# Optimization experiments

Hardware: AMD Instinct MI355X
Metric: run time of the kernel (lower is better)

Reference implementation:

```python
import jax, jax.numpy as jnp
import numpy as np

DIM = 512
N_HEADS = 8
HEAD_DIM = DIM // N_HEADS
TAU = 0.5
LN_EPS = 1e-5
B, L = 16, 8192


def setup_inputs() -> dict:
    key = jax.random.key(0)
    ks = jax.random.split(key, 12)
    s = 1.0 / np.sqrt(DIM)
    return {
        "Q": jax.random.normal(ks[0], (B, DIM), jnp.float32),
        "K": jax.random.normal(ks[1], (B, L, DIM), jnp.float32),
        "V": jax.random.normal(ks[2], (B, L, DIM), jnp.float32),
        "Wq": jax.random.normal(ks[3], (DIM, DIM), jnp.float32) * s,
        "bq": jnp.zeros((DIM,), jnp.float32),
        "Wk": jax.random.normal(ks[4], (DIM, DIM), jnp.float32) * s,
        "bk": jnp.zeros((DIM,), jnp.float32),
        "Wv": jax.random.normal(ks[5], (DIM, DIM), jnp.float32) * s,
        "bv": jnp.zeros((DIM,), jnp.float32),
        "Wo": jax.random.normal(ks[6], (DIM, DIM), jnp.float32) * s,
        "bo": jnp.zeros((DIM,), jnp.float32),
        "gamma": jnp.ones((DIM,), jnp.float32),
        "beta": jnp.zeros((DIM,), jnp.float32),
    }


def _layer_norm(x, gamma, beta):
    mu = jnp.mean(x, axis=-1, keepdims=True)
    var = jnp.var(x, axis=-1, keepdims=True)
    return (x - mu) * jax.lax.rsqrt(var + LN_EPS) * gamma + beta


def reference(Q, K, V, Wq, bq, Wk, bk, Wv, bv, Wo, bo, gamma, beta):
    Bsz = Q.shape[0]
    # projections
    q = (Q @ Wq + bq).reshape(Bsz, N_HEADS, HEAD_DIM)            # b h d
    k = (K @ Wk + bk).reshape(Bsz, -1, N_HEADS, HEAD_DIM)        # b l h d
    v = (V @ Wv + bv).reshape(Bsz, -1, N_HEADS, HEAD_DIM)        # b l h d
    # scaled dot-product score: single query per head
    scores = jnp.einsum("bhd,blhd->bhl", q, k) / np.sqrt(HEAD_DIM)
    # 'exp' simplex projection = temperature softmax
    weights = jax.nn.softmax(scores / TAU, axis=-1)              # b h l
    ctx = jnp.einsum("bhl,blhd->bhd", weights, v).reshape(Bsz, DIM)
    out = ctx @ Wo + bo                                          # n_heads != 1
    out = _layer_norm(out, gamma, beta)
    return out + Q
```

## Files before the change

kernel.cpp:

```cpp
#include <hip/hip_runtime.h>
#include <math.h>

#define DIM 512
#define NH 8
#define HD 64
#define LSEQ 8192
#define BSZ 16


__global__ __launch_bounds__(256) void k_qproj(const float* __restrict__ Q,
        const float* __restrict__ Wq, const float* __restrict__ bq,
        float* __restrict__ q) {
    int b = blockIdx.x >> 1;
    int j = ((blockIdx.x & 1) << 8) + threadIdx.x;
    __shared__ float qs[DIM];
    qs[threadIdx.x]       = Q[b * DIM + threadIdx.x];
    qs[threadIdx.x + 256] = Q[b * DIM + threadIdx.x + 256];
    __syncthreads();
    float acc = bq[j];
    #pragma unroll 8
    for (int i = 0; i < DIM; ++i) acc = fmaf(qs[i], Wq[i * DIM + j], acc);
    q[b * DIM + j] = acc;
}

__global__ __launch_bounds__(256) void k_tproj(const float* __restrict__ q,
        const float* __restrict__ Wk, float* __restrict__ t) {
    int b = blockIdx.x >> 4;
    int o = ((blockIdx.x & 15) << 8) + threadIdx.x;
    int h = o >> 9, i = o & 511;
    __shared__ float qs[DIM];
    qs[threadIdx.x]       = q[b * DIM + threadIdx.x];
    qs[threadIdx.x + 256] = q[b * DIM + threadIdx.x + 256];
    __syncthreads();
    const float* wk = Wk + (size_t)i * DIM + h * HD;
    const float* qh = qs + h * HD;
    float a = 0.f;
    #pragma unroll
    for (int j = 0; j < HD; ++j) a = fmaf(wk[j], qh[j], a);
    t[(b * NH + h) * DIM + i] = 0.25f * a;
}

__global__ __launch_bounds__(256) void k_scores(const float* __restrict__ Kin,
        const float* __restrict__ t, float* __restrict__ sc) {
    int b  = blockIdx.x >> 8;
    int l0 = (blockIdx.x & 255) << 5;
    int lane = threadIdx.x & 63;
    int wave = threadIdx.x >> 6;
    float4 ta[NH], tb[NH];
    #pragma unroll
    for (int h = 0; h < NH; ++h) {
        const float* tp = t + (b * NH + h) * DIM + lane * 8;
        ta[h] = *(const float4*)tp;
        tb[h] = *(const float4*)(tp + 4);
    }
    int lbase = l0 + wave * 8;
    float keep = 0.f;
    #pragma unroll
    for (int i = 0; i < 8; ++i) {
        const float* kp = Kin + ((size_t)(b * LSEQ + lbase + i)) * DIM + lane * 8;
        float4 ka = *(const float4*)kp;
        float4 kb = *(const float4*)(kp + 4);
        float s[NH];
        #pragma unroll
        for (int h = 0; h < NH; ++h) {
            float p = ka.x * ta[h].x + ka.y * ta[h].y + ka.z * ta[h].z + ka.w * ta[h].w
                    + kb.x * tb[h].x + kb.y * tb[h].y + kb.z * tb[h].z + kb.w * tb[h].w;
            p += __shfl_xor(p, 1);
            p += __shfl_xor(p, 2);
            p += __shfl_xor(p, 4);
            p += __shfl_xor(p, 8);
            p += __shfl_xor(p, 16);
            p += __shfl_xor(p, 32);
            s[h] = p;
        }
        int hh = lane >> 3;
        float sel = s[0];
        sel = (hh == 1) ? s[1] : sel;
        sel = (hh == 2) ? s[2] : sel;
        sel = (hh == 3) ? s[3] : sel;
        sel = (hh == 4) ? s[4] : sel;
        sel = (hh == 5) ? s[5] : sel;
        sel = (hh == 6) ? s[6] : sel;
        sel = (hh == 7) ? s[7] : sel;
        if ((lane & 7) == i) keep = sel;
    }
    int h = lane >> 3, i = lane & 7;
    sc[(size_t)(b * NH + h) * LSEQ + lbase + i] = keep;
}

__global__ __launch_bounds__(256) void k_softmax(float* __restrict__ sc) {
    float* base = sc + (size_t)blockIdx.x * LSEQ;
    int tid = threadIdx.x;
    int lane = tid & 63, wave = tid >> 6;
    float4 v[8];
    float m = -1e30f;
    #pragma unroll
    for (int k = 0; k < 8; ++k) {
        v[k] = *(const float4*)(base + tid * 4 + k * 1024);
        m = fmaxf(m, fmaxf(fmaxf(v[k].x, v[k].y), fmaxf(v[k].z, v[k].w)));
    }
    #pragma unroll
    for (int d = 1; d < 64; d <<= 1) m = fmaxf(m, __shfl_xor(m, d));
    __shared__ float sm[4], ss[4];
    if (lane == 0) sm[wave] = m;
    __syncthreads();
    m = fmaxf(fmaxf(sm[0], sm[1]), fmaxf(sm[2], sm[3]));
    float sum = 0.f;
    #pragma unroll
    for (int k = 0; k < 8; ++k) {
        v[k].x = __expf(v[k].x - m);
        v[k].y = __expf(v[k].y - m);
        v[k].z = __expf(v[k].z - m);
        v[k].w = __expf(v[k].w - m);
        sum += v[k].x + v[k].y + v[k].z + v[k].w;
    }
    #pragma unroll
    for (int d = 1; d < 64; d <<= 1) sum += __shfl_xor(sum, d);
    if (lane == 0) ss[wave] = sum;
    __syncthreads();
    sum = ss[0] + ss[1] + ss[2] + ss[3];
    float inv = 1.f / sum;
    #pragma unroll
    for (int k = 0; k < 8; ++k) {
        v[k].x *= inv; v[k].y *= inv; v[k].z *= inv; v[k].w *= inv;
        *(float4*)(base + tid * 4 + k * 1024) = v[k];
    }
}

__global__ __launch_bounds__(256) void k_vpass(const float* __restrict__ Vin,
        const float* __restrict__ sc, float* __restrict__ part) {
    int b = blockIdx.x >> 5;
    int chunk = blockIdx.x & 31;
    int l0 = chunk << 8;
    int tid = threadIdx.x;
    __shared__ float smem[4096];
    #pragma unroll
    for (int idx = tid; idx < 2048; idx += 256) {
        int h = idx >> 8, j = idx & 255;
        smem[j * 8 + h] = sc[(size_t)(b * NH + h) * LSEQ + l0 + j];
    }
    __syncthreads();
    int r = tid >> 7;
    int col = (tid & 127) << 2;
    float4 a0 = {0,0,0,0}, a1 = {0,0,0,0}, a2 = {0,0,0,0}, a3 = {0,0,0,0};
    float4 a4 = {0,0,0,0}, a5 = {0,0,0,0}, a6 = {0,0,0,0}, a7 = {0,0,0,0};
    #pragma unroll 4
    for (int j = r; j < 256; j += 2) {
        const float* vp = Vin + ((size_t)(b * LSEQ + l0 + j)) * DIM + col;
        float4 vv = *(const float4*)vp;
        float4 wa = *(const float4*)&smem[j * 8];
        float4 wb = *(const float4*)&smem[j * 8 + 4];
        a0.x = fmaf(wa.x, vv.x, a0.x); a0.y = fmaf(wa.x, vv.y, a0.y);
        a0.z = fmaf(wa.x, vv.z, a0.z); a0.w = fmaf(wa.x, vv.w, a0.w);
        a1.x = fmaf(wa.y, vv.x, a1.x); a1.y = fmaf(wa.y, vv.y, a1.y);
        a1.z = fmaf(wa.y, vv.z, a1.z); a1.w = fmaf(wa.y, vv.w, a1.w);
        a2.x = fmaf(wa.z, vv.x, a2.x); a2.y = fmaf(wa.z, vv.y, a2.y);
        a2.z = fmaf(wa.z, vv.z, a2.z); a2.w = fmaf(wa.z, vv.w, a2.w);
        a3.x = fmaf(wa.w, vv.x, a3.x); a3.y = fmaf(wa.w, vv.y, a3.y);
        a3.z = fmaf(wa.w, vv.z, a3.z); a3.w = fmaf(wa.w, vv.w, a3.w);
        a4.x = fmaf(wb.x, vv.x, a4.x); a4.y = fmaf(wb.x, vv.y, a4.y);
        a4.z = fmaf(wb.x, vv.z, a4.z); a4.w = fmaf(wb.x, vv.w, a4.w);
        a5.x = fmaf(wb.y, vv.x, a5.x); a5.y = fmaf(wb.y, vv.y, a5.y);
        a5.z = fmaf(wb.y, vv.z, a5.z); a5.w = fmaf(wb.y, vv.w, a5.w);
        a6.x = fmaf(wb.z, vv.x, a6.x); a6.y = fmaf(wb.z, vv.y, a6.y);
        a6.z = fmaf(wb.z, vv.z, a6.z); a6.w = fmaf(wb.z, vv.w, a6.w);
        a7.x = fmaf(wb.w, vv.x, a7.x); a7.y = fmaf(wb.w, vv.y, a7.y);
        a7.z = fmaf(wb.w, vv.z, a7.z); a7.w = fmaf(wb.w, vv.w, a7.w);
    }
    __syncthreads();
    if (r == 1) {
        *(float4*)&smem[0 * DIM + col] = a0; *(float4*)&smem[1 * DIM + col] = a1;
        *(float4*)&smem[2 * DIM + col] = a2; *(float4*)&smem[3 * DIM + col] = a3;
        *(float4*)&smem[4 * DIM + col] = a4; *(float4*)&smem[5 * DIM + col] = a5;
        *(float4*)&smem[6 * DIM + col] = a6; *(float4*)&smem[7 * DIM + col] = a7;
    }
    __syncthreads();
    if (r == 0) {
        float* pout = part + (size_t)(b * 32 + chunk) * 4096;
        float4 o;
        #define EMIT(H, A) \
            o = *(const float4*)&smem[H * DIM + col]; \
            o.x += A.x; o.y += A.y; o.z += A.z; o.w += A.w; \
            *(float4*)&pout[H * DIM + col] = o;
        EMIT(0, a0) EMIT(1, a1) EMIT(2, a2) EMIT(3, a3)
        EMIT(4, a4) EMIT(5, a5) EMIT(6, a6) EMIT(7, a7)
        #undef EMIT
    }
}

__global__ __launch_bounds__(256) void k_ureduce(const float* __restrict__ part,
        float* __restrict__ u) {
    int o = blockIdx.x * 256 + threadIdx.x;
    int b = o >> 12, rr = o & 4095;
    float s = 0.f;
    #pragma unroll 8
    for (int c = 0; c < 32; ++c) s += part[(size_t)(b * 32 + c) * 4096 + rr];
    u[o] = s;
}

__global__ __launch_bounds__(256) void k_ctx(const float* __restrict__ u,
        const float* __restrict__ Wv, const float* __restrict__ bv,
        float* __restrict__ ctx) {
    int b = blockIdx.x >> 1;
    int j = ((blockIdx.x & 1) << 8) + threadIdx.x;
    __shared__ float us[4096];
    for (int idx = threadIdx.x; idx < 4096; idx += 256) us[idx] = u[b * 4096 + idx];
    __syncthreads();
    int h = j >> 6;
    const float* uh = us + h * DIM;
    float a = bv[j];
    #pragma unroll 8
    for (int i = 0; i < DIM; ++i) a = fmaf(uh[i], Wv[(size_t)i * DIM + j], a);
    ctx[b * DIM + j] = a;
}

__global__ __launch_bounds__(256) void k_out(const float* __restrict__ ctx,
        const float* __restrict__ Wo, const float* __restrict__ bo,
        const float* __restrict__ gamma, const float* __restrict__ beta,
        const float* __restrict__ Qin, float* __restrict__ out) {
    int b = blockIdx.x;
    int tid = threadIdx.x;
    __shared__ float cs[DIM];
    cs[tid]       = ctx[b * DIM + tid];
    cs[tid + 256] = ctx[b * DIM + tid + 256];
    __syncthreads();
    float o0 = bo[tid], o1 = bo[tid + 256];
    #pragma unroll 8
    for (int m = 0; m < DIM; ++m) {
        float c = cs[m];
        o0 = fmaf(c, Wo[m * DIM + tid], o0);
        o1 = fmaf(c, Wo[m * DIM + tid + 256], o1);
    }
    float s = o0 + o1, sq = o0 * o0 + o1 * o1;
    #pragma unroll
    for (int d = 1; d < 64; d <<= 1) { s += __shfl_xor(s, d); sq += __shfl_xor(sq, d); }
    __shared__ float rs[4], rq[4];
    int lane = tid & 63, wave = tid >> 6;
    if (lane == 0) { rs[wave] = s; rq[wave] = sq; }
    __syncthreads();
    s  = rs[0] + rs[1] + rs[2] + rs[3];
    sq = rq[0] + rq[1] + rq[2] + rq[3];
    float mu = s * (1.f / DIM);
    float var = sq * (1.f / DIM) - mu * mu;
    float rstd = rsqrtf(var + 1e-5f);
    int j0 = tid, j1 = tid + 256;
    out[b * DIM + j0] = (o0 - mu) * rstd * gamma[j0] + beta[j0] + Qin[b * DIM + j0];
    out[b * DIM + j1] = (o1 - mu) * rstd * gamma[j1] + beta[j1] + Qin[b * DIM + j1];
}

extern "C" void kernel_launch(void* const* d_in, const int* in_sizes, int n_in,
                              void* d_out, int out_size, void* d_ws, size_t ws_size,
                              hipStream_t stream) {
    const float* Q     = (const float*)d_in[0];
    const float* K     = (const float*)d_in[1];
    const float* V     = (const float*)d_in[2];
    const float* Wq    = (const float*)d_in[3];
    const float* bq    = (const float*)d_in[4];
    const float* Wk    = (const float*)d_in[5];
    const float* Wv    = (const float*)d_in[7];
    const float* bv    = (const float*)d_in[8];
    const float* Wo    = (const float*)d_in[9];
    const float* bo    = (const float*)d_in[10];
    const float* gamma = (const float*)d_in[11];
    const float* beta  = (const float*)d_in[12];
    float* ws   = (float*)d_ws;
    float* q    = ws;
    float* t    = ws + 8192;
    float* sc   = ws + 73728;
    float* part = ws + 1122304;
    float* u    = ws + 3219456;
    float* ctx  = ws + 3284992;
    float* out  = (float*)d_out;

    k_qproj  <<<32,   256, 0, stream>>>(Q, Wq, bq, q);
    k_tproj  <<<256,  256, 0, stream>>>(q, Wk, t);
    k_scores <<<4096, 256, 0, stream>>>(K, t, sc);
    k_softmax<<<128,  256, 0, stream>>>(sc);
    k_vpass  <<<512,  256, 0, stream>>>(V, sc, part);
    k_ureduce<<<256,  256, 0, stream>>>(part, u);
    k_ctx    <<<32,   256, 0, stream>>>(u, Wv, bv, ctx);
    k_out    <<<16,   256, 0, stream>>>(ctx, Wo, bo, gamma, beta, Q, out);
}
```

Baseline: 643.4 us.

## Fuse scores, softmax and V pass into one flash-style attention kernel

Merges score computation, softmax and the weighted V sum into a single kernel per 128-row chunk. Each chunk keeps its local max and sum, and a later kernel rescales and combines the chunks. This removes the score round-trip to global memory and several launches. The Q and T projections are fused per (batch, head), and the output projection is split over K-slices with a separate LayerNorm kernel to expose more parallelism. Risks include fewer blocks in the attention kernel and the extra partial storage and merge cost.

```diff
diff --git a/kernel.cpp b/kernel.cpp
--- a/kernel.cpp
+++ b/kernel.cpp
@@ -6,150 +6,136 @@
 #define HD 64
 #define LSEQ 8192
 #define BSZ 16
-
-
-__global__ __launch_bounds__(256) void k_qproj(const float* __restrict__ Q,
+#define CHUNK 128
+#define NCH 64
+#define PSTRIDE 4112
+
+
+__global__ __launch_bounds__(256) void k_qt(const float* __restrict__ Q,
         const float* __restrict__ Wq, const float* __restrict__ bq,
-        float* __restrict__ q) {
-    int b = blockIdx.x >> 1;
-    int j = ((blockIdx.x & 1) << 8) + threadIdx.x;
-    __shared__ float qs[DIM];
-    qs[threadIdx.x]       = Q[b * DIM + threadIdx.x];
-    qs[threadIdx.x + 256] = Q[b * DIM + threadIdx.x + 256];
-    __syncthreads();
-    float acc = bq[j];
-    #pragma unroll 8
-    for (int i = 0; i < DIM; ++i) acc = fmaf(qs[i], Wq[i * DIM + j], acc);
-    q[b * DIM + j] = acc;
-}
-
-__global__ __launch_bounds__(256) void k_tproj(const float* __restrict__ q,
-        const float* __restrict__ Wk, float* __restrict__ t) {
-    int b = blockIdx.x >> 4;
-    int o = ((blockIdx.x & 15) << 8) + threadIdx.x;
-    int h = o >> 9, i = o & 511;
-    __shared__ float qs[DIM];
-    qs[threadIdx.x]       = q[b * DIM + threadIdx.x];
-    qs[threadIdx.x + 256] = q[b * DIM + threadIdx.x + 256];
-    __syncthreads();
-    const float* wk = Wk + (size_t)i * DIM + h * HD;
-    const float* qh = qs + h * HD;
-    float a = 0.f;
+        const float* __restrict__ Wk, float* __restrict__ t_g) {
+    int b = blockIdx.x >> 3, h = blockIdx.x & 7;
+    int tid = threadIdx.x;
+    __shared__ __align__(16) float qs[DIM];
+    __shared__ __align__(16) float partial[256];
+    __shared__ __align__(16) float qh[HD];
+    qs[tid]       = Q[b * DIM + tid];
+    qs[tid + 256] = Q[b * DIM + tid + 256];
+    __syncthreads();
+    int jj = tid & 63, ks = tid >> 6;
+    {
+        float a = 0.f;
+        const float* wp = Wq + (size_t)(ks * 128) * DIM + h * HD + jj;
+        const float* qp = qs + ks * 128;
+        #pragma unroll 8
+        for (int i = 0; i < 128; ++i) a = fmaf(qp[i], wp[(size_t)i * DIM], a);
+        partial[tid] = a;
+    }
+    __syncthreads();
+    if (tid < 64)
+        qh[tid] = partial[tid] + partial[tid + 64] + partial[tid + 128] +
+                  partial[tid + 192] + bq[h * HD + tid];
+    __syncthreads();
     #pragma unroll
-    for (int j = 0; j < HD; ++j) a = fmaf(wk[j], qh[j], a);
-    t[(b * NH + h) * DIM + i] = 0.25f * a;
-}
-
-__global__ __launch_bounds__(256) void k_scores(const float* __restrict__ Kin,
-        const float* __restrict__ t, float* __restrict__ sc) {
-    int b  = blockIdx.x >> 8;
-    int l0 = (blockIdx.x & 255) << 5;
-    int lane = threadIdx.x & 63;
-    int wave = threadIdx.x >> 6;
-    float4 ta[NH], tb[NH];
+    for (int rep = 0; rep < 2; ++rep) {
+        int i = tid + rep * 256;
+        const float4* wk = (const float4*)(Wk + (size_t)i * DIM + h * HD);
+        float a = 0.f;
+        #pragma unroll
+        for (int v = 0; v < 16; ++v) {
+            float4 w4 = wk[v];
+            a = fmaf(w4.x, qh[v * 4 + 0], a);
+            a = fmaf(w4.y, qh[v * 4 + 1], a);
+            a = fmaf(w4.z, qh[v * 4 + 2], a);
+            a = fmaf(w4.w, qh[v * 4 + 3], a);
+        }
+        t_g[(size_t)(b * NH + h) * DIM + i] = 0.25f * a;
+    }
+}
+
+__global__ __launch_bounds__(256) void k_attn(const float* __restrict__ Kin,
+        const float* __restrict__ Vin, const float* __restrict__ t_g,
+        float* __restrict__ part) {
+    int b = blockIdx.x >> 6, chunk = blockIdx.x & 63;
+    int tid = threadIdx.x, lane = tid & 63, w = tid >> 6;
+    __shared__ __align__(16) float e_lds[CHUNK * 8];
+    __shared__ __align__(16) float vstage[8 * DIM];
+    __shared__ float wred[32];
+    __shared__ float wsum[32];
+    float4 ta[8], tb[8];
     #pragma unroll
-    for (int h = 0; h < NH; ++h) {
-        const float* tp = t + (b * NH + h) * DIM + lane * 8;
+    for (int h = 0; h < 8; ++h) {
+        const float* tp = t_g + (size_t)(b * NH + h) * DIM + lane * 8;
         ta[h] = *(const float4*)tp;
         tb[h] = *(const float4*)(tp + 4);
     }
-    int lbase = l0 + wave * 8;
-    float keep = 0.f;
-    #pragma unroll
-    for (int i = 0; i < 8; ++i) {
-        const float* kp = Kin + ((size_t)(b * LSEQ + lbase + i)) * DIM + lane * 8;
-        float4 ka = *(const float4*)kp;
-        float4 kb = *(const float4*)(kp + 4);
-        float s[NH];
+    const size_t rowbase = (size_t)(b * LSEQ + chunk * CHUNK);
+    for (int g = 0; g < 4; ++g) {
+        int r0 = w * 32 + g * 8;
+        float keep = 0.f;
         #pragma unroll
-        for (int h = 0; h < NH; ++h) {
-            float p = ka.x * ta[h].x + ka.y * ta[h].y + ka.z * ta[h].z + ka.w * ta[h].w
-                    + kb.x * tb[h].x + kb.y * tb[h].y + kb.z * tb[h].z + kb.w * tb[h].w;
-            p += __shfl_xor(p, 1);
-            p += __shfl_xor(p, 2);
-            p += __shfl_xor(p, 4);
-            p += __shfl_xor(p, 8);
-            p += __shfl_xor(p, 16);
-            p += __shfl_xor(p, 32);
-            s[h] = p;
+        for (int i = 0; i < 8; ++i) {
+            const float* kp = Kin + (rowbase + r0 + i) * DIM + lane * 8;
+            float4 ka = *(const float4*)kp;
+            float4 kb = *(const float4*)(kp + 4);
+            float s[8];
+            #pragma unroll
+            for (int h = 0; h < 8; ++h) {
+                float p = ka.x * ta[h].x + ka.y * ta[h].y + ka.z * ta[h].z + ka.w * ta[h].w
+                        + kb.x * tb[h].x + kb.y * tb[h].y + kb.z * tb[h].z + kb.w * tb[h].w;
+                p += __shfl_xor(p, 1);
+                p += __shfl_xor(p, 2);
+                p += __shfl_xor(p, 4);
+                p += __shfl_xor(p, 8);
+                p += __shfl_xor(p, 16);
+                p += __shfl_xor(p, 32);
+                s[h] = p;
+            }
+            int hh = lane >> 3;
+            float sel = s[0];
+            sel = (hh == 1) ? s[1] : sel;
+            sel = (hh == 2) ? s[2] : sel;
+            sel = (hh == 3) ? s[3] : sel;
+            sel = (hh == 4) ? s[4] : sel;
+            sel = (hh == 5) ? s[5] : sel;
+            sel = (hh == 6) ? s[6] : sel;
+            sel = (hh == 7) ? s[7] : sel;
+            if ((lane & 7) == i) keep = sel;
         }
-        int hh = lane >> 3;
-        float sel = s[0];
-        sel = (hh == 1) ? s[1] : sel;
-        sel = (hh == 2) ? s[2] : sel;
-        sel = (hh == 3) ? s[3] : sel;
-        sel = (hh == 4) ? s[4] : sel;
-        sel = (hh == 5) ? s[5] : sel;
-        sel = (hh == 6) ? s[6] : sel;
-        sel = (hh == 7) ? s[7] : sel;
-        if ((lane & 7) == i) keep = sel;
-    }
-    int h = lane >> 3, i = lane & 7;
-    sc[(size_t)(b * NH + h) * LSEQ + lbase + i] = keep;
-}
-
-__global__ __launch_bounds__(256) void k_softmax(float* __restrict__ sc) {
-    float* base = sc + (size_t)blockIdx.x * LSEQ;
-    int tid = threadIdx.x;
-    int lane = tid & 63, wave = tid >> 6;
-    float4 v[8];
-    float m = -1e30f;
-    #pragma unroll
-    for (int k = 0; k < 8; ++k) {
-        v[k] = *(const float4*)(base + tid * 4 + k * 1024);
-        m = fmaxf(m, fmaxf(fmaxf(v[k].x, v[k].y), fmaxf(v[k].z, v[k].w)));
-    }
-    #pragma unroll
-    for (int d = 1; d < 64; d <<= 1) m = fmaxf(m, __shfl_xor(m, d));
-    __shared__ float sm[4], ss[4];
-    if (lane == 0) sm[wave] = m;
-    __syncthreads();
-    m = fmaxf(fmaxf(sm[0], sm[1]), fmaxf(sm[2], sm[3]));
-    float sum = 0.f;
-    #pragma unroll
-    for (int k = 0; k < 8; ++k) {
-        v[k].x = __expf(v[k].x - m);
-        v[k].y = __expf(v[k].y - m);
-        v[k].z = __expf(v[k].z - m);
-        v[k].w = __expf(v[k].w - m);
-        sum += v[k].x + v[k].y + v[k].z + v[k].w;
-    }
-    #pragma unroll
-    for (int d = 1; d < 64; d <<= 1) sum += __shfl_xor(sum, d);
-    if (lane == 0) ss[wave] = sum;
-    __syncthreads();
-    sum = ss[0] + ss[1] + ss[2] + ss[3];
-    float inv = 1.f / sum;
-    #pragma unroll
-    for (int k = 0; k < 8; ++k) {
-        v[k].x *= inv; v[k].y *= inv; v[k].z *= inv; v[k].w *= inv;
-        *(float4*)(base + tid * 4 + k * 1024) = v[k];
-    }
-}
-
-__global__ __launch_bounds__(256) void k_vpass(const float* __restrict__ Vin,
-        const float* __restrict__ sc, float* __restrict__ part) {
-    int b = blockIdx.x >> 5;
-    int chunk = blockIdx.x & 31;
-    int l0 = chunk << 8;
-    int tid = threadIdx.x;
-    __shared__ float smem[4096];
-    #pragma unroll
-    for (int idx = tid; idx < 2048; idx += 256) {
-        int h = idx >> 8, j = idx & 255;
-        smem[j * 8 + h] = sc[(size_t)(b * NH + h) * LSEQ + l0 + j];
-    }
-    __syncthreads();
-    int r = tid >> 7;
-    int col = (tid & 127) << 2;
+        e_lds[(r0 + (lane & 7)) * 8 + (lane >> 3)] = keep;
+    }
+    __syncthreads();
+    int h2 = tid & 7, rb = (tid >> 3) * 4;
+    float x0 = e_lds[(rb + 0) * 8 + h2], x1 = e_lds[(rb + 1) * 8 + h2];
+    float x2 = e_lds[(rb + 2) * 8 + h2], x3 = e_lds[(rb + 3) * 8 + h2];
+    float mx = fmaxf(fmaxf(x0, x1), fmaxf(x2, x3));
+    mx = fmaxf(mx, __shfl_xor(mx, 8));
+    mx = fmaxf(mx, __shfl_xor(mx, 16));
+    mx = fmaxf(mx, __shfl_xor(mx, 32));
+    if (lane < 8) wred[w * 8 + lane] = mx;
+    __syncthreads();
+    float m = fmaxf(fmaxf(wred[h2], wred[8 + h2]), fmaxf(wred[16 + h2], wred[24 + h2]));
+    float e0 = __expf(x0 - m), e1 = __expf(x1 - m);
+    float e2 = __expf(x2 - m), e3 = __expf(x3 - m);
+    e_lds[(rb + 0) * 8 + h2] = e0;
+    e_lds[(rb + 1) * 8 + h2] = e1;
+    e_lds[(rb + 2) * 8 + h2] = e2;
+    e_lds[(rb + 3) * 8 + h2] = e3;
+    float sm = e0 + e1 + e2 + e3;
+    sm += __shfl_xor(sm, 8);
+    sm += __shfl_xor(sm, 16);
+    sm += __shfl_xor(sm, 32);
+    if (lane < 8) wsum[w * 8 + lane] = sm;
+    __syncthreads();
+    int r = tid >> 7, col = (tid & 127) << 2;
     float4 a0 = {0,0,0,0}, a1 = {0,0,0,0}, a2 = {0,0,0,0}, a3 = {0,0,0,0};
     float4 a4 = {0,0,0,0}, a5 = {0,0,0,0}, a6 = {0,0,0,0}, a7 = {0,0,0,0};
     #pragma unroll 4
-    for (int j = r; j < 256; j += 2) {
-        const float* vp = Vin + ((size_t)(b * LSEQ + l0 + j)) * DIM + col;
+    for (int j = r; j < CHUNK; j += 2) {
+        const float* vp = Vin + (rowbase + j) * DIM + col;
         float4 vv = *(const float4*)vp;
-        float4 wa = *(const float4*)&smem[j * 8];
-        float4 wb = *(const float4*)&smem[j * 8 + 4];
+        float4 wa = *(const float4*)&e_lds[j * 8];
+        float4 wb = *(const float4*)&e_lds[j * 8 + 4];
         a0.x = fmaf(wa.x, vv.x, a0.x); a0.y = fmaf(wa.x, vv.y, a0.y);
         a0.z = fmaf(wa.x, vv.z, a0.z); a0.w = fmaf(wa.x, vv.w, a0.w);
         a1.x = fmaf(wa.y, vv.x, a1.x); a1.y = fmaf(wa.y, vv.y, a1.y);
@@ -169,67 +155,107 @@
     }
     __syncthreads();
     if (r == 1) {
-        *(float4*)&smem[0 * DIM + col] = a0; *(float4*)&smem[1 * DIM + col] = a1;
-        *(float4*)&smem[2 * DIM + col] = a2; *(float4*)&smem[3 * DIM + col] = a3;
-        *(float4*)&smem[4 * DIM + col] = a4; *(float4*)&smem[5 * DIM + col] = a5;
-        *(float4*)&smem[6 * DIM + col] = a6; *(float4*)&smem[7 * DIM + col] = a7;
-    }
-    __syncthreads();
+        *(float4*)&vstage[0 * DIM + col] = a0; *(float4*)&vstage[1 * DIM + col] = a1;
+        *(float4*)&vstage[2 * DIM + col] = a2; *(float4*)&vstage[3 * DIM + col] = a3;
+        *(float4*)&vstage[4 * DIM + col] = a4; *(float4*)&vstage[5 * DIM + col] = a5;
+        *(float4*)&vstage[6 * DIM + col] = a6; *(float4*)&vstage[7 * DIM + col] = a7;
+    }
+    __syncthreads();
+    float* pout = part + (size_t)(b * NCH + chunk) * PSTRIDE;
     if (r == 0) {
-        float* pout = part + (size_t)(b * 32 + chunk) * 4096;
         float4 o;
         #define EMIT(H, A) \
-            o = *(const float4*)&smem[H * DIM + col]; \
+            o = *(const float4*)&vstage[H * DIM + col]; \
             o.x += A.x; o.y += A.y; o.z += A.z; o.w += A.w; \
             *(float4*)&pout[H * DIM + col] = o;
         EMIT(0, a0) EMIT(1, a1) EMIT(2, a2) EMIT(3, a3)
         EMIT(4, a4) EMIT(5, a5) EMIT(6, a6) EMIT(7, a7)
         #undef EMIT
     }
-}
-
-__global__ __launch_bounds__(256) void k_ureduce(const float* __restrict__ part,
-        float* __restrict__ u) {
-    int o = blockIdx.x * 256 + threadIdx.x;
-    int b = o >> 12, rr = o & 4095;
-    float s = 0.f;
-    #pragma unroll 8
-    for (int c = 0; c < 32; ++c) s += part[(size_t)(b * 32 + c) * 4096 + rr];
-    u[o] = s;
-}
-
-__global__ __launch_bounds__(256) void k_ctx(const float* __restrict__ u,
+    if (tid < 8) {
+        float mm = fmaxf(fmaxf(wred[tid], wred[8 + tid]), fmaxf(wred[16 + tid], wred[24 + tid]));
+        pout[4096 + tid] = mm;
+        pout[4104 + tid] = wsum[tid] + wsum[8 + tid] + wsum[16 + tid] + wsum[24 + tid];
+    }
+}
+
+__global__ __launch_bounds__(256) void k_uctx(const float* __restrict__ part,
         const float* __restrict__ Wv, const float* __restrict__ bv,
         float* __restrict__ ctx) {
-    int b = blockIdx.x >> 1;
-    int j = ((blockIdx.x & 1) << 8) + threadIdx.x;
-    __shared__ float us[4096];
-    for (int idx = threadIdx.x; idx < 4096; idx += 256) us[idx] = u[b * 4096 + idx];
-    __syncthreads();
-    int h = j >> 6;
-    const float* uh = us + h * DIM;
-    float a = bv[j];
+    int b = blockIdx.x >> 3, h = blockIdx.x & 7;
+    int tid = threadIdx.x;
+    __shared__ __align__(16) float alphas[NCH];
+    __shared__ __align__(16) float u_lds[DIM];
+    __shared__ __align__(16) float red4[256];
+    __shared__ float sinv_s;
+    if (tid < 64) {
+        const float* pm = part + (size_t)(b * NCH + tid) * PSTRIDE;
+        float mv = pm[4096 + h], sv = pm[4104 + h];
+        float M = mv;
+        #pragma unroll
+        for (int d = 1; d < 64; d <<= 1) M = fmaxf(M, __shfl_xor(M, d));
+        float al = __expf(mv - M);
+        alphas[tid] = al;
+        float c = al * sv;
+        #pragma unroll
+        for (int d = 1; d < 64; d <<= 1) c += __shfl_xor(c, d);
+        if (tid == 0) sinv_s = 1.f / c;
+    }
+    __syncthreads();
+    float sinv = sinv_s;
+    float u0 = 0.f, u1 = 0.f;
+    #pragma unroll 4
+    for (int c = 0; c < NCH; ++c) {
+        const float* pu = part + (size_t)(b * NCH + c) * PSTRIDE + h * DIM;
+        float al = alphas[c];
+        u0 = fmaf(al, pu[tid], u0);
+        u1 = fmaf(al, pu[tid + 256], u1);
+    }
+    u_lds[tid]       = u0 * sinv;
+    u_lds[tid + 256] = u1 * sinv;
+    __syncthreads();
+    int jj = tid & 63, ks = tid >> 6;
+    float a = 0.f;
+    const float* wp = Wv + (size_t)(ks * 128) * DIM + h * HD + jj;
+    const float* up = u_lds + ks * 128;
     #pragma unroll 8
-    for (int i = 0; i < DIM; ++i) a = fmaf(uh[i], Wv[(size_t)i * DIM + j], a);
-    ctx[b * DIM + j] = a;
-}
-
-__global__ __launch_bounds__(256) void k_out(const float* __restrict__ ctx,
-        const float* __restrict__ Wo, const float* __restrict__ bo,
-        const float* __restrict__ gamma, const float* __restrict__ beta,
-        const float* __restrict__ Qin, float* __restrict__ out) {
-    int b = blockIdx.x;
+    for (int i = 0; i < 128; ++i) a = fmaf(up[i], wp[(size_t)i * DIM], a);
+    red4[tid] = a;
+    __syncthreads();
+    if (tid < 64)
+        ctx[b * DIM + h * HD + tid] = red4[tid] + red4[tid + 64] +
+            red4[tid + 128] + red4[tid + 192] + bv[h * HD + tid];
+}
+
+__global__ __launch_bounds__(256) void k_oproj(const float* __restrict__ ctx,
+        const float* __restrict__ Wo, float* __restrict__ po) {
+    int b = blockIdx.x >> 3, ks = blockIdx.x & 7;
     int tid = threadIdx.x;
-    __shared__ float cs[DIM];
-    cs[tid]       = ctx[b * DIM + tid];
-    cs[tid + 256] = ctx[b * DIM + tid + 256];
-    __syncthreads();
+    __shared__ float cs[64];
+    if (tid < 64) cs[tid] = ctx[b * DIM + ks * 64 + tid];
+    __syncthreads();
+    float a0 = 0.f, a1 = 0.f;
+    const float* wp = Wo + (size_t)(ks * 64) * DIM;
+    #pragma unroll 8
+    for (int i = 0; i < 64; ++i) {
+        float c = cs[i];
+        a0 = fmaf(c, wp[(size_t)i * DIM + tid], a0);
+        a1 = fmaf(c, wp[(size_t)i * DIM + tid + 256], a1);
+    }
+    po[(size_t)(b * 8 + ks) * DIM + tid]       = a0;
+    po[(size_t)(b * 8 + ks) * DIM + tid + 256] = a1;
+}
+
+__global__ __launch_bounds__(256) void k_ln(const float* __restrict__ po,
+        const float* __restrict__ bo, const float* __restrict__ gamma,
+        const float* __restrict__ beta, const float* __restrict__ Qin,
+        float* __restrict__ out) {
+    int b = blockIdx.x, tid = threadIdx.x;
     float o0 = bo[tid], o1 = bo[tid + 256];
-    #pragma unroll 8
-    for (int m = 0; m < DIM; ++m) {
-        float c = cs[m];
-        o0 = fmaf(c, Wo[m * DIM + tid], o0);
-        o1 = fmaf(c, Wo[m * DIM + tid + 256], o1);
+    #pragma unroll
+    for (int ks = 0; ks < 8; ++ks) {
+        o0 += po[(size_t)(b * 8 + ks) * DIM + tid];
+        o1 += po[(size_t)(b * 8 + ks) * DIM + tid + 256];
     }
     float s = o0 + o1, sq = o0 * o0 + o1 * o1;
     #pragma unroll
@@ -264,20 +290,15 @@
     const float* gamma = (const float*)d_in[11];
     const float* beta  = (const float*)d_in[12];
     float* ws   = (float*)d_ws;
-    float* q    = ws;
-    float* t    = ws + 8192;
-    float* sc   = ws + 73728;
-    float* part = ws + 1122304;
-    float* u    = ws + 3219456;
-    float* ctx  = ws + 3284992;
+    float* t_g  = ws;
+    float* part = ws + 65536;
+    float* ctx  = ws + 4276224;
+    float* po   = ws + 4284416;
     float* out  = (float*)d_out;
 
-    k_qproj  <<<32,   256, 0, stream>>>(Q, Wq, bq, q);
-    k_tproj  <<<256,  256, 0, stream>>>(q, Wk, t);
-    k_scores <<<4096, 256, 0, stream>>>(K, t, sc);
-    k_softmax<<<128,  256, 0, stream>>>(sc);
-    k_vpass  <<<512,  256, 0, stream>>>(V, sc, part);
-    k_ureduce<<<256,  256, 0, stream>>>(part, u);
-    k_ctx    <<<32,   256, 0, stream>>>(u, Wv, bv, ctx);
-    k_out    <<<16,   256, 0, stream>>>(ctx, Wo, bo, gamma, beta, Q, out);
-}
+    k_qt   <<<128,  256, 0, stream>>>(Q, Wq, bq, Wk, t_g);
+    k_attn <<<1024, 256, 0, stream>>>(K, V, t_g, part);
+    k_uctx <<<128,  256, 0, stream>>>(part, Wv, bv, ctx);
+    k_oproj<<<128,  256, 0, stream>>>(ctx, Wo, po);
+    k_ln   <<<16,   256, 0, stream>>>(po, bo, gamma, beta, Q, out);
+}
```

Measured after the change: 574.6 us. -10.7%, faster.
